# Optimization experiments

Hardware: AMD Instinct MI355X
Metric: run time of the kernel (lower is better)

Reference implementation:

```python
import jax, jax.numpy as jnp
import numpy as np

BITS = 8
TOPK_PERCENT = 0.1
THRESHOLD = 0.5


def _quantize_per_channel(v, n_bits):
    # scales: abs-max over last dim, clamped, divided by q_max
    q_max = 2 ** (n_bits - 1) - 1
    scales = jnp.max(jnp.abs(v), axis=-1, keepdims=True)
    scales = jnp.clip(scales, 1e-5, None) / q_max
    return jnp.clip(jnp.round(v / scales), -q_max - 1, q_max) * scales


def setup_inputs() -> dict:
    key = jax.random.key(0)
    ks = jax.random.split(key, 5)
    B, S, D, H = 4, 2048, 1024, 4096
    return {
        "x": jax.random.normal(ks[0], (B, S, D), dtype=jnp.float32),
        "W1": jax.random.normal(ks[1], (H, D), dtype=jnp.float32) * 0.02,
        "b1": jax.random.normal(ks[2], (H,), dtype=jnp.float32) * 0.02,
        "W2": jax.random.normal(ks[3], (D, H), dtype=jnp.float32) * 0.02,
        "b2": jax.random.normal(ks[4], (D,), dtype=jnp.float32) * 0.02,
    }


def reference(x, W1, b1, W2, b2):
    D = W1.shape[-1]
    H = W1.shape[0]
    topk_rows = int(D * TOPK_PERCENT) + 1  # first-k-columns approximation

    # approximate preactivation using only the first topk_rows input channels
    prod_topk = jnp.einsum('bsk,hk->bsh', x[:, :, :topk_rows], W1[:, :topk_rows]) + b1
    # exact fp preactivation
    prod = jnp.einsum('bsd,hd->bsh', x, W1) + b1

    # quantized path: per-channel quant of x, W1, b1 then matmul
    q_x = _quantize_per_channel(x, BITS)
    q_w = _quantize_per_channel(W1, BITS)
    q_b = _quantize_per_channel(b1, BITS)
    q_pre = jnp.einsum('bsd,hd->bsh', q_x, q_w) + q_b

    # channel selection: channels predicted positive often enough stay fp
    threshold = prod_topk.shape[-1] * THRESHOLD
    num_pos_pred = jnp.sum(prod_topk > 0, axis=(0, 1))  # [H]
    fp_channels = num_pos_pred > threshold              # [H] bool

    h = jnp.where(fp_channels, prod, q_pre)
    h = jax.nn.gelu(h, approximate=False)
    out = jnp.einsum('bsh,dh->bsd', h, W2) + b2
    return out
```

## Files before the change

### kernel.cpp

```cpp
#include <hip/hip_runtime.h>
#include <math.h>
#include <stdint.h>


typedef __bf16 v8bf __attribute__((ext_vector_type(8)));
typedef float v4f __attribute__((ext_vector_type(4)));
typedef unsigned short v8us __attribute__((ext_vector_type(8)));

#define AS_G __attribute__((address_space(1)))
#define AS_L __attribute__((address_space(3)))

__device__ __forceinline__ unsigned short f2bf(float f) {
    union { float f; unsigned int i; } v; v.f = f;
    unsigned int r = v.i + 0x7fffu + ((v.i >> 16) & 1u);
    return (unsigned short)(r >> 16);
}
__device__ __forceinline__ float gelu_fast(float v) {
    float u = v * (0.79788456080286536f + 0.035677408136300125f * v * v);
    u = fminf(fmaxf(u, -15.f), 15.f);
    float e = __expf(2.0f * u);
    return v * e * __builtin_amdgcn_rcpf(e + 1.0f);
}
__device__ __forceinline__ float gelu_exact(float v) {
    return 0.5f * v * (1.0f + erff(v * 0.70710678118654752440f));
}

__device__ __forceinline__ void gemm_core(const unsigned short* __restrict__ A,
                                          const unsigned short* __restrict__ B,
                                          int K, int bm0, int bn0,
                                          unsigned short* lds,
                                          v4f acc[4][4])
{
    const int tid  = threadIdx.x;
    const int wave = tid >> 6;
    const int lane = tid & 63;
    const int rowInChunk = lane >> 2;
    const int col8 = ((lane & 3) ^ ((lane >> 3) & 3)) * 8;
    const int ldsLane = lane * 8;
    const int c0 = wave * 2, c1 = wave * 2 + 1;
    const int wm = wave & 1, wn = wave >> 1;

    unsigned short* ldsA = lds;
    unsigned short* ldsB = lds + 4096;

    const size_t aR0 = (size_t)(bm0 + c0 * 16 + rowInChunk) * K + col8;
    const size_t aR1 = (size_t)(bm0 + c1 * 16 + rowInChunk) * K + col8;
    const size_t bR0 = (size_t)(bn0 + c0 * 16 + rowInChunk) * K + col8;
    const size_t bR1 = (size_t)(bn0 + c1 * 16 + rowInChunk) * K + col8;

    const int R = lane & 15, Q = lane >> 4;
    const int roff = R * 32 + ((Q ^ ((R >> 1) & 3)) * 8);

    for (int k0 = 0; k0 < K; k0 += 32) {
        __builtin_amdgcn_global_load_lds((const AS_G void*)(A + aR0 + k0),
                                         (AS_L void*)(ldsA + c0 * 512 + ldsLane), 16, 0, 0);
        __builtin_amdgcn_global_load_lds((const AS_G void*)(A + aR1 + k0),
                                         (AS_L void*)(ldsA + c1 * 512 + ldsLane), 16, 0, 0);
        __builtin_amdgcn_global_load_lds((const AS_G void*)(B + bR0 + k0),
                                         (AS_L void*)(ldsB + c0 * 512 + ldsLane), 16, 0, 0);
        __builtin_amdgcn_global_load_lds((const AS_G void*)(B + bR1 + k0),
                                         (AS_L void*)(ldsB + c1 * 512 + ldsLane), 16, 0, 0);
        __syncthreads();

        v8bf af[4], bfr[4];
#pragma unroll
        for (int i = 0; i < 4; ++i)
            af[i] = *(const v8bf*)&ldsA[(wm * 4 + i) * 512 + roff];
#pragma unroll
        for (int j = 0; j < 4; ++j)
            bfr[j] = *(const v8bf*)&ldsB[(wn * 4 + j) * 512 + roff];
#pragma unroll
        for (int i = 0; i < 4; ++i)
#pragma unroll
            for (int j = 0; j < 4; ++j)
                acc[i][j] = __builtin_amdgcn_mfma_f32_16x16x32_bf16(af[i], bfr[j], acc[i][j], 0, 0, 0);
        __syncthreads();
    }
}

__device__ __forceinline__ void gemm_core64N(const unsigned short* __restrict__ A,
                                             const unsigned short* __restrict__ B,
                                             int K, int bm0, int bn0,
                                             unsigned short* lds,
                                             v4f acc[4][2])
{
    const int tid  = threadIdx.x;
    const int wave = tid >> 6;
    const int lane = tid & 63;
    const int rowInChunk = lane >> 2;
    const int col8 = ((lane & 3) ^ ((lane >> 3) & 3)) * 8;
    const int ldsLane = lane * 8;
    const int c0 = wave * 2, c1 = wave * 2 + 1;
    const int wm = wave & 1, wn = wave >> 1;

    unsigned short* ldsA = lds;
    unsigned short* ldsB = lds + 4096;

    const size_t aR0 = (size_t)(bm0 + c0 * 16 + rowInChunk) * K + col8;
    const size_t aR1 = (size_t)(bm0 + c1 * 16 + rowInChunk) * K + col8;
    const size_t bR  = (size_t)(bn0 + wave * 16 + rowInChunk) * K + col8;

    const int R = lane & 15, Q = lane >> 4;
    const int roff = R * 32 + ((Q ^ ((R >> 1) & 3)) * 8);

    for (int k0 = 0; k0 < K; k0 += 32) {
        __builtin_amdgcn_global_load_lds((const AS_G void*)(A + aR0 + k0),
                                         (AS_L void*)(ldsA + c0 * 512 + ldsLane), 16, 0, 0);
        __builtin_amdgcn_global_load_lds((const AS_G void*)(A + aR1 + k0),
                                         (AS_L void*)(ldsA + c1 * 512 + ldsLane), 16, 0, 0);
        __builtin_amdgcn_global_load_lds((const AS_G void*)(B + bR + k0),
                                         (AS_L void*)(ldsB + wave * 512 + ldsLane), 16, 0, 0);
        __syncthreads();

        v8bf af[4], bfr[2];
#pragma unroll
        for (int i = 0; i < 4; ++i)
            af[i] = *(const v8bf*)&ldsA[(wm * 4 + i) * 512 + roff];
#pragma unroll
        for (int j = 0; j < 2; ++j)
            bfr[j] = *(const v8bf*)&ldsB[(wn * 2 + j) * 512 + roff];
#pragma unroll
        for (int i = 0; i < 4; ++i)
#pragma unroll
            for (int j = 0; j < 2; ++j)
                acc[i][j] = __builtin_amdgcn_mfma_f32_16x16x32_bf16(af[i], bfr[j], acc[i][j], 0, 0, 0);
        __syncthreads();
    }
}

__global__ void prep_kernel(const float* __restrict__ x, const float* __restrict__ W1,
                            const float* __restrict__ W2, const float* __restrict__ b1,
                            unsigned short* __restrict__ xb, unsigned short* __restrict__ w1b,
                            unsigned short* __restrict__ w2b,
                            unsigned short* __restrict__ xpad, unsigned short* __restrict__ w1pad,
                            float* __restrict__ s_x, float* __restrict__ s_w,
                            float* __restrict__ s_b, int* __restrict__ counts)
{
    const int b = blockIdx.x, t = threadIdx.x;
    __shared__ float red[4];

    if (b < 16384) {
        const float* src; unsigned short* dst; unsigned short* pad = nullptr; float* sc = nullptr;
        if (b < 8192)       { src = x  + (size_t)b * 1024;            dst = xb  + (size_t)b * 1024;
                              pad = xpad  + (size_t)b * 128;          sc = s_x + b; }
        else if (b < 12288) { int r = b - 8192;  src = W1 + (size_t)r * 1024; dst = w1b + (size_t)r * 1024;
                              pad = w1pad + (size_t)r * 128;          sc = s_w + r; }
        else                { int r = b - 12288; src = W2 + (size_t)r * 1024; dst = w2b + (size_t)r * 1024; }

        float4 v = ((const float4*)src)[t];
        ushort4 u;
        u.x = f2bf(v.x); u.y = f2bf(v.y); u.z = f2bf(v.z); u.w = f2bf(v.w);
        ((ushort4*)dst)[t] = u;
        if (pad && t < 32) {
            int c = t * 4;
            ushort4 p;
            p.x = (c + 0 < 103) ? u.x : (unsigned short)0;
            p.y = (c + 1 < 103) ? u.y : (unsigned short)0;
            p.z = (c + 2 < 103) ? u.z : (unsigned short)0;
            p.w = (c + 3 < 103) ? u.w : (unsigned short)0;
            ((ushort4*)pad)[t] = p;
        }
        if (sc) {
            float m = fmaxf(fmaxf(fabsf(v.x), fabsf(v.y)), fmaxf(fabsf(v.z), fabsf(v.w)));
#pragma unroll
            for (int off = 32; off; off >>= 1) m = fmaxf(m, __shfl_xor(m, off, 64));
            if ((t & 63) == 0) red[t >> 6] = m;
            __syncthreads();
            if (t == 0) {
                m = fmaxf(fmaxf(red[0], red[1]), fmaxf(red[2], red[3]));
                *sc = fmaxf(m, 1e-5f) * (1.0f / 127.0f);
            }
        }
    } else {
        float m = 0.f;
        for (int k = t; k < 4096; k += 256) { m = fmaxf(m, fabsf(b1[k])); counts[k] = 0; }
#pragma unroll
        for (int off = 32; off; off >>= 1) m = fmaxf(m, __shfl_xor(m, off, 64));
        if ((t & 63) == 0) red[t >> 6] = m;
        __syncthreads();
        if (t == 0) {
            m = fmaxf(fmaxf(red[0], red[1]), fmaxf(red[2], red[3]));
            *s_b = fmaxf(m, 1e-5f) * (1.0f / 127.0f);
        }
    }
}

__global__ __launch_bounds__(256, 4)
void gemm1_topk(const unsigned short* __restrict__ xb,
                const unsigned short* __restrict__ w1b,
                const unsigned short* __restrict__ xpad,
                const unsigned short* __restrict__ w1pad,
                const float* __restrict__ b1,
                unsigned short* __restrict__ hbuf,
                int* __restrict__ counts)
{
    __shared__ unsigned short lds[8192];
    v4f acc[4][4];
    v4f z = {0.f, 0.f, 0.f, 0.f};
#pragma unroll
    for (int i = 0; i < 4; ++i)
#pragma unroll
        for (int j = 0; j < 4; ++j) acc[i][j] = z;

    const int bm0 = blockIdx.x * 128, bn0 = blockIdx.y * 128;
    const int tid = threadIdx.x;
    const int lane = tid & 63, wave = tid >> 6;
    const int wm = wave & 1, wn = wave >> 1, q = lane >> 4;

    if (blockIdx.z == 0) {
        gemm_core(xb, w1b, 1024, bm0, bn0, lds, acc);

        float bvj[4];
#pragma unroll
        for (int j = 0; j < 4; ++j) bvj[j] = b1[bn0 + wn * 64 + j * 16 + (lane & 15)];

#pragma unroll
        for (int p = 0; p < 2; ++p) {
            __syncthreads();
            if (wm == p) {
#pragma unroll
                for (int j = 0; j < 4; ++j) {
                    int nl = wn * 64 + j * 16 + (lane & 15);
#pragma unroll
                    for (int i = 0; i < 4; ++i)
#pragma unroll
                        for (int r = 0; r < 4; ++r)
                            lds[(i * 16 + q * 4 + r) * 128 + nl] =
                                f2bf(gelu_fast(acc[i][j][r] + bvj[j]));
                }
            }
            __syncthreads();
#pragma unroll
            for (int s = 0; s < 4; ++s) {
                int c = s * 256 + tid;
                int row = c >> 4, ch = c & 15;
                *(v8us*)&hbuf[(size_t)(bm0 + p * 64 + row) * 4096 + bn0 + ch * 8] =
                    *(const v8us*)&lds[row * 128 + ch * 8];
            }
        }
    } else {
        gemm_core(xpad, w1pad, 128, bm0, bn0, lds, acc);

#pragma unroll
        for (int j = 0; j < 4; ++j) {
            int n = bn0 + wn * 64 + j * 16 + (lane & 15);
            float bv = b1[n];
            int cnt = 0;
#pragma unroll
            for (int i = 0; i < 4; ++i)
#pragma unroll
                for (int r = 0; r < 4; ++r)
                    cnt += (acc[i][j][r] + bv > 0.0f) ? 1 : 0;
            cnt += __shfl_xor(cnt, 16, 64);
            cnt += __shfl_xor(cnt, 32, 64);
            if (lane < 16 && cnt) atomicAdd(&counts[n], cnt);
        }
    }
}

__global__ void fixup_kernel(const float* __restrict__ x,
                             const float* __restrict__ W1,
                             const float* __restrict__ b1,
                             const int* __restrict__ counts,
                             const float* __restrict__ s_x,
                             const float* __restrict__ s_w,
                             const float* __restrict__ s_b,
                             unsigned short* __restrict__ hbuf)
{
    const int n = blockIdx.x;
    if (counts[n] > 2048) return;
    __shared__ float qw[1024];
    const float swn = s_w[n];
    for (int k = threadIdx.x; k < 1024; k += 256) {
        float q = nearbyintf(W1[(size_t)n * 1024 + k] / swn);
        qw[k] = fminf(fmaxf(q, -128.f), 127.f) * swn;
    }
    __syncthreads();
    const float sb = *s_b;
    const float bq = fminf(fmaxf(nearbyintf(b1[n] / sb), -128.f), 127.f) * sb;
    for (int m = threadIdx.x; m < 8192; m += 256) {
        const float sxm = s_x[m];
        float a = 0.f;
        for (int k = 0; k < 1024; ++k) {
            float q = nearbyintf(x[(size_t)m * 1024 + k] / sxm);
            a += fminf(fmaxf(q, -128.f), 127.f) * sxm * qw[k];
        }
        hbuf[(size_t)m * 4096 + n] = f2bf(gelu_exact(a + bq));
    }
}

__global__ __launch_bounds__(256, 4)
void gemm2_bias(const unsigned short* __restrict__ hbuf,
                const unsigned short* __restrict__ w2b,
                const float* __restrict__ b2,
                float* __restrict__ out)
{
    __shared__ unsigned short lds[6144];
    v4f acc[4][2];
    v4f z = {0.f, 0.f, 0.f, 0.f};
#pragma unroll
    for (int i = 0; i < 4; ++i)
#pragma unroll
        for (int j = 0; j < 2; ++j) acc[i][j] = z;

    const int bm0 = blockIdx.x * 128, bn0 = blockIdx.y * 64;
    gemm_core64N(hbuf, w2b, 4096, bm0, bn0, lds, acc);

    const int tid = threadIdx.x;
    const int lane = tid & 63, wave = tid >> 6;
    const int wm = wave & 1, wn = wave >> 1, q = lane >> 4;
    float* ldsf = (float*)lds;

    float bvj[2];
#pragma unroll
    for (int j = 0; j < 2; ++j) bvj[j] = b2[bn0 + wn * 32 + j * 16 + (lane & 15)];

#pragma unroll
    for (int p = 0; p < 4; ++p) {
        __syncthreads();
        if (wm == (p >> 1)) {
            const int ibase = (p & 1) * 2;
#pragma unroll
            for (int ii = 0; ii < 2; ++ii) {
#pragma unroll
                for (int j = 0; j < 2; ++j) {
                    int nl = wn * 32 + j * 16 + (lane & 15);
#pragma unroll
                    for (int r = 0; r < 4; ++r)
                        ldsf[(ii * 16 + q * 4 + r) * 64 + nl] =
                            acc[ibase + ii][j][r] + bvj[j];
                }
            }
        }
        __syncthreads();
#pragma unroll
        for (int s = 0; s < 2; ++s) {
            int c = s * 256 + tid;
            int row = c >> 4, ch = c & 15;
            *(float4*)&out[(size_t)(bm0 + p * 32 + row) * 1024 + bn0 + ch * 4] =
                *(const float4*)&ldsf[row * 64 + ch * 4];
        }
    }
}

extern "C" void kernel_launch(void* const* d_in, const int* in_sizes, int n_in,
                              void* d_out, int out_size, void* d_ws, size_t ws_size,
                              hipStream_t stream)
{
    const float* x  = (const float*)d_in[0];
    const float* W1 = (const float*)d_in[1];
    const float* b1 = (const float*)d_in[2];
    const float* W2 = (const float*)d_in[3];
    const float* b2 = (const float*)d_in[4];
    float* out = (float*)d_out;

    unsigned short* xb  = (unsigned short*)d_out;
    unsigned short* w1b = (unsigned short*)d_out + (size_t)8192 * 1024;

    char* ws = (char*)d_ws;
    int*   counts = (int*)(ws + 0);
    float* s_x    = (float*)(ws + (64 << 10));
    float* s_w    = (float*)(ws + (96 << 10));
    float* s_b    = (float*)(ws + (112 << 10));
    unsigned short* xpad  = (unsigned short*)(ws + (1 << 20));
    unsigned short* w1pad = (unsigned short*)(ws + (3 << 20));
    unsigned short* w2b   = (unsigned short*)(ws + (4 << 20));
    unsigned short* hbuf  = (unsigned short*)(ws + (12 << 20));

    prep_kernel<<<16385, 256, 0, stream>>>(x, W1, W2, b1, xb, w1b, w2b,
                                           xpad, w1pad, s_x, s_w, s_b, counts);
    gemm1_topk<<<dim3(64, 32, 2), 256, 0, stream>>>(xb, w1b, xpad, w1pad, b1, hbuf, counts);
    fixup_kernel<<<4096, 256, 0, stream>>>(x, W1, b1, counts, s_x, s_w, s_b, hbuf);
    gemm2_bias<<<dim3(64, 16), 256, 0, stream>>>(hbuf, w2b, b2, out);
}
```

Baseline: 299.3 us.

## Move W2 bf16 conversion into gemm1 grid and split fixup over row chunks

The W2 fp32-to-bf16 conversion moves out of the prep kernel into an extra z-slice of the gemm1 launch, so it can overlap with the GEMM blocks and prep gets shorter. The fixup kernel grid gains a second dimension that splits the 8192 rows into 8 chunks, giving more parallel blocks for the rare quantized channels. This also drops the branch on pad and scale pointers in prep. It adds lightweight blocks to gemm1 that compete with the GEMM blocks for CU slots, and fixup now reloads the quantized W1 row once per chunk.

```diff
diff --git a/kernel.cpp b/kernel.cpp
--- a/kernel.cpp
+++ b/kernel.cpp
@@ -129,9 +129,8 @@
 }
 
 __global__ void prep_kernel(const float* __restrict__ x, const float* __restrict__ W1,
-                            const float* __restrict__ W2, const float* __restrict__ b1,
+                            const float* __restrict__ b1,
                             unsigned short* __restrict__ xb, unsigned short* __restrict__ w1b,
-                            unsigned short* __restrict__ w2b,
                             unsigned short* __restrict__ xpad, unsigned short* __restrict__ w1pad,
                             float* __restrict__ s_x, float* __restrict__ s_w,
                             float* __restrict__ s_b, int* __restrict__ counts)
@@ -139,19 +138,18 @@
     const int b = blockIdx.x, t = threadIdx.x;
     __shared__ float red[4];
 
-    if (b < 16384) {
-        const float* src; unsigned short* dst; unsigned short* pad = nullptr; float* sc = nullptr;
-        if (b < 8192)       { src = x  + (size_t)b * 1024;            dst = xb  + (size_t)b * 1024;
-                              pad = xpad  + (size_t)b * 128;          sc = s_x + b; }
-        else if (b < 12288) { int r = b - 8192;  src = W1 + (size_t)r * 1024; dst = w1b + (size_t)r * 1024;
-                              pad = w1pad + (size_t)r * 128;          sc = s_w + r; }
-        else                { int r = b - 12288; src = W2 + (size_t)r * 1024; dst = w2b + (size_t)r * 1024; }
+    if (b < 12288) {
+        const float* src; unsigned short* dst; unsigned short* pad; float* sc;
+        if (b < 8192) { src = x  + (size_t)b * 1024;            dst = xb  + (size_t)b * 1024;
+                        pad = xpad  + (size_t)b * 128;          sc = s_x + b; }
+        else          { int r = b - 8192;  src = W1 + (size_t)r * 1024; dst = w1b + (size_t)r * 1024;
+                        pad = w1pad + (size_t)r * 128;          sc = s_w + r; }
 
         float4 v = ((const float4*)src)[t];
         ushort4 u;
         u.x = f2bf(v.x); u.y = f2bf(v.y); u.z = f2bf(v.z); u.w = f2bf(v.w);
         ((ushort4*)dst)[t] = u;
-        if (pad && t < 32) {
+        if (t < 32) {
             int c = t * 4;
             ushort4 p;
             p.x = (c + 0 < 103) ? u.x : (unsigned short)0;
@@ -160,16 +158,14 @@
             p.w = (c + 3 < 103) ? u.w : (unsigned short)0;
             ((ushort4*)pad)[t] = p;
         }
-        if (sc) {
-            float m = fmaxf(fmaxf(fabsf(v.x), fabsf(v.y)), fmaxf(fabsf(v.z), fabsf(v.w)));
-#pragma unroll
-            for (int off = 32; off; off >>= 1) m = fmaxf(m, __shfl_xor(m, off, 64));
-            if ((t & 63) == 0) red[t >> 6] = m;
-            __syncthreads();
-            if (t == 0) {
-                m = fmaxf(fmaxf(red[0], red[1]), fmaxf(red[2], red[3]));
-                *sc = fmaxf(m, 1e-5f) * (1.0f / 127.0f);
-            }
+        float m = fmaxf(fmaxf(fabsf(v.x), fabsf(v.y)), fmaxf(fabsf(v.z), fabsf(v.w)));
+#pragma unroll
+        for (int off = 32; off; off >>= 1) m = fmaxf(m, __shfl_xor(m, off, 64));
+        if ((t & 63) == 0) red[t >> 6] = m;
+        __syncthreads();
+        if (t == 0) {
+            m = fmaxf(fmaxf(red[0], red[1]), fmaxf(red[2], red[3]));
+            *sc = fmaxf(m, 1e-5f) * (1.0f / 127.0f);
         }
     } else {
         float m = 0.f;
@@ -191,10 +187,28 @@
                 const unsigned short* __restrict__ xpad,
                 const unsigned short* __restrict__ w1pad,
                 const float* __restrict__ b1,
+                const float* __restrict__ W2,
+                unsigned short* __restrict__ w2b,
                 unsigned short* __restrict__ hbuf,
                 int* __restrict__ counts)
 {
     __shared__ unsigned short lds[8192];
+    const int tid = threadIdx.x;
+
+    if (blockIdx.z == 2) {
+        const int r = (blockIdx.y * 64 + (int)blockIdx.x) * 2;
+        const float* src = W2 + (size_t)r * 1024;
+        unsigned short* dst = w2b + (size_t)r * 1024;
+#pragma unroll
+        for (int h = 0; h < 2; ++h) {
+            float4 v = ((const float4*)src)[tid + h * 256];
+            ushort4 u;
+            u.x = f2bf(v.x); u.y = f2bf(v.y); u.z = f2bf(v.z); u.w = f2bf(v.w);
+            ((ushort4*)dst)[tid + h * 256] = u;
+        }
+        return;
+    }
+
     v4f acc[4][4];
     v4f z = {0.f, 0.f, 0.f, 0.f};
 #pragma unroll
@@ -203,7 +217,6 @@
         for (int j = 0; j < 4; ++j) acc[i][j] = z;
 
     const int bm0 = blockIdx.x * 128, bn0 = blockIdx.y * 128;
-    const int tid = threadIdx.x;
     const int lane = tid & 63, wave = tid >> 6;
     const int wm = wave & 1, wn = wave >> 1, q = lane >> 4;
 
@@ -278,7 +291,8 @@
     __syncthreads();
     const float sb = *s_b;
     const float bq = fminf(fmaxf(nearbyintf(b1[n] / sb), -128.f), 127.f) * sb;
-    for (int m = threadIdx.x; m < 8192; m += 256) {
+    const int m0 = blockIdx.y * 1024;
+    for (int m = m0 + threadIdx.x; m < m0 + 1024; m += 256) {
         const float sxm = s_x[m];
         float a = 0.f;
         for (int k = 0; k < 1024; ++k) {
@@ -367,9 +381,10 @@
     unsigned short* w2b   = (unsigned short*)(ws + (4 << 20));
     unsigned short* hbuf  = (unsigned short*)(ws + (12 << 20));
 
-    prep_kernel<<<16385, 256, 0, stream>>>(x, W1, W2, b1, xb, w1b, w2b,
+    prep_kernel<<<12289, 256, 0, stream>>>(x, W1, b1, xb, w1b,
                                            xpad, w1pad, s_x, s_w, s_b, counts);
-    gemm1_topk<<<dim3(64, 32, 2), 256, 0, stream>>>(xb, w1b, xpad, w1pad, b1, hbuf, counts);
-    fixup_kernel<<<4096, 256, 0, stream>>>(x, W1, b1, counts, s_x, s_w, s_b, hbuf);
+    gemm1_topk<<<dim3(64, 32, 3), 256, 0, stream>>>(xb, w1b, xpad, w1pad, b1,
+                                                    W2, w2b, hbuf, counts);
+    fixup_kernel<<<dim3(4096, 8), 256, 0, stream>>>(x, W1, b1, counts, s_x, s_w, s_b, hbuf);
     gemm2_bias<<<dim3(64, 16), 256, 0, stream>>>(hbuf, w2b, b2, out);
 }
```

New measurement: 317.8 us. 6.2% more time.

## Double-buffer LDS in both GEMM cores to overlap global loads with MFMA

Applied to the files above, without the earlier changes.

Both GEMM inner loops now use two LDS stages. The next K-tile is issued via global_load_lds into the alternate buffer before the current tile's MFMAs run, which removes one of the two barriers per iteration. The MFMA block is wrapped in s_setprio to favor math waves. This doubles the LDS per block (32KB and 24KB), which may limit occupancy under launch_bounds(256,4). It also depends on the single remaining barrier being enough to order the async LDS writes correctly.

```diff
diff --git a/kernel.cpp b/kernel.cpp
--- a/kernel.cpp
+++ b/kernel.cpp
@@ -9,6 +9,7 @@
 
 #define AS_G __attribute__((address_space(1)))
 #define AS_L __attribute__((address_space(3)))
+#define GLOAD(gp, lp) __builtin_amdgcn_global_load_lds((const AS_G void*)(gp), (AS_L void*)(lp), 16, 0, 0)
 
 __device__ __forceinline__ unsigned short f2bf(float f) {
     union { float f; unsigned int i; } v; v.f = f;
@@ -40,9 +41,6 @@
     const int c0 = wave * 2, c1 = wave * 2 + 1;
     const int wm = wave & 1, wn = wave >> 1;
 
-    unsigned short* ldsA = lds;
-    unsigned short* ldsB = lds + 4096;
-
     const size_t aR0 = (size_t)(bm0 + c0 * 16 + rowInChunk) * K + col8;
     const size_t aR1 = (size_t)(bm0 + c1 * 16 + rowInChunk) * K + col8;
     const size_t bR0 = (size_t)(bn0 + c0 * 16 + rowInChunk) * K + col8;
@@ -50,32 +48,40 @@
 
     const int R = lane & 15, Q = lane >> 4;
     const int roff = R * 32 + ((Q ^ ((R >> 1) & 3)) * 8);
-
-    for (int k0 = 0; k0 < K; k0 += 32) {
-        __builtin_amdgcn_global_load_lds((const AS_G void*)(A + aR0 + k0),
-                                         (AS_L void*)(ldsA + c0 * 512 + ldsLane), 16, 0, 0);
-        __builtin_amdgcn_global_load_lds((const AS_G void*)(A + aR1 + k0),
-                                         (AS_L void*)(ldsA + c1 * 512 + ldsLane), 16, 0, 0);
-        __builtin_amdgcn_global_load_lds((const AS_G void*)(B + bR0 + k0),
-                                         (AS_L void*)(ldsB + c0 * 512 + ldsLane), 16, 0, 0);
-        __builtin_amdgcn_global_load_lds((const AS_G void*)(B + bR1 + k0),
-                                         (AS_L void*)(ldsB + c1 * 512 + ldsLane), 16, 0, 0);
-        __syncthreads();
+    const int NT = K >> 5;
+
+#define G1_STG(t, bp) { const int kk_ = (t) << 5;                              \
+        GLOAD(A + aR0 + kk_, (bp) + c0 * 512 + ldsLane);                       \
+        GLOAD(A + aR1 + kk_, (bp) + c1 * 512 + ldsLane);                       \
+        GLOAD(B + bR0 + kk_, (bp) + 4096 + c0 * 512 + ldsLane);                \
+        GLOAD(B + bR1 + kk_, (bp) + 4096 + c1 * 512 + ldsLane); }
+
+    G1_STG(0, lds);
+    __syncthreads();
+
+    for (int t = 0; t < NT; ++t) {
+        unsigned short* cur = lds + (t & 1) * 8192;
+        unsigned short* nxt = lds + ((t + 1) & 1) * 8192;
+        if (t + 1 < NT) { G1_STG(t + 1, nxt); }
+        __builtin_amdgcn_sched_barrier(0);
 
         v8bf af[4], bfr[4];
 #pragma unroll
         for (int i = 0; i < 4; ++i)
-            af[i] = *(const v8bf*)&ldsA[(wm * 4 + i) * 512 + roff];
+            af[i] = *(const v8bf*)&cur[(wm * 4 + i) * 512 + roff];
 #pragma unroll
         for (int j = 0; j < 4; ++j)
-            bfr[j] = *(const v8bf*)&ldsB[(wn * 4 + j) * 512 + roff];
+            bfr[j] = *(const v8bf*)&cur[4096 + (wn * 4 + j) * 512 + roff];
+        __builtin_amdgcn_s_setprio(1);
 #pragma unroll
         for (int i = 0; i < 4; ++i)
 #pragma unroll
             for (int j = 0; j < 4; ++j)
                 acc[i][j] = __builtin_amdgcn_mfma_f32_16x16x32_bf16(af[i], bfr[j], acc[i][j], 0, 0, 0);
-        __syncthreads();
-    }
+        __builtin_amdgcn_s_setprio(0);
+        __syncthreads();
+    }
+#undef G1_STG
 }
 
 __device__ __forceinline__ void gemm_core64N(const unsigned short* __restrict__ A,
@@ -93,39 +99,45 @@
     const int c0 = wave * 2, c1 = wave * 2 + 1;
     const int wm = wave & 1, wn = wave >> 1;
 
-    unsigned short* ldsA = lds;
-    unsigned short* ldsB = lds + 4096;
-
     const size_t aR0 = (size_t)(bm0 + c0 * 16 + rowInChunk) * K + col8;
     const size_t aR1 = (size_t)(bm0 + c1 * 16 + rowInChunk) * K + col8;
     const size_t bR  = (size_t)(bn0 + wave * 16 + rowInChunk) * K + col8;
 
     const int R = lane & 15, Q = lane >> 4;
     const int roff = R * 32 + ((Q ^ ((R >> 1) & 3)) * 8);
-
-    for (int k0 = 0; k0 < K; k0 += 32) {
-        __builtin_amdgcn_global_load_lds((const AS_G void*)(A + aR0 + k0),
-                                         (AS_L void*)(ldsA + c0 * 512 + ldsLane), 16, 0, 0);
-        __builtin_amdgcn_global_load_lds((const AS_G void*)(A + aR1 + k0),
-                                         (AS_L void*)(ldsA + c1 * 512 + ldsLane), 16, 0, 0);
-        __builtin_amdgcn_global_load_lds((const AS_G void*)(B + bR + k0),
-                                         (AS_L void*)(ldsB + wave * 512 + ldsLane), 16, 0, 0);
-        __syncthreads();
+    const int NT = K >> 5;
+
+#define G2_STG(t, bp) { const int kk_ = (t) << 5;                              \
+        GLOAD(A + aR0 + kk_, (bp) + c0 * 512 + ldsLane);                       \
+        GLOAD(A + aR1 + kk_, (bp) + c1 * 512 + ldsLane);                       \
+        GLOAD(B + bR  + kk_, (bp) + 4096 + wave * 512 + ldsLane); }
+
+    G2_STG(0, lds);
+    __syncthreads();
+
+    for (int t = 0; t < NT; ++t) {
+        unsigned short* cur = lds + (t & 1) * 6144;
+        unsigned short* nxt = lds + ((t + 1) & 1) * 6144;
+        if (t + 1 < NT) { G2_STG(t + 1, nxt); }
+        __builtin_amdgcn_sched_barrier(0);
 
         v8bf af[4], bfr[2];
 #pragma unroll
         for (int i = 0; i < 4; ++i)
-            af[i] = *(const v8bf*)&ldsA[(wm * 4 + i) * 512 + roff];
+            af[i] = *(const v8bf*)&cur[(wm * 4 + i) * 512 + roff];
 #pragma unroll
         for (int j = 0; j < 2; ++j)
-            bfr[j] = *(const v8bf*)&ldsB[(wn * 2 + j) * 512 + roff];
+            bfr[j] = *(const v8bf*)&cur[4096 + (wn * 2 + j) * 512 + roff];
+        __builtin_amdgcn_s_setprio(1);
 #pragma unroll
         for (int i = 0; i < 4; ++i)
 #pragma unroll
             for (int j = 0; j < 2; ++j)
                 acc[i][j] = __builtin_amdgcn_mfma_f32_16x16x32_bf16(af[i], bfr[j], acc[i][j], 0, 0, 0);
-        __syncthreads();
-    }
+        __builtin_amdgcn_s_setprio(0);
+        __syncthreads();
+    }
+#undef G2_STG
 }
 
 __global__ void prep_kernel(const float* __restrict__ x, const float* __restrict__ W1,
@@ -194,7 +206,7 @@
                 unsigned short* __restrict__ hbuf,
                 int* __restrict__ counts)
 {
-    __shared__ unsigned short lds[8192];
+    __shared__ unsigned short lds[16384];
     v4f acc[4][4];
     v4f z = {0.f, 0.f, 0.f, 0.f};
 #pragma unroll
@@ -295,7 +307,7 @@
                 const float* __restrict__ b2,
                 float* __restrict__ out)
 {
-    __shared__ unsigned short lds[6144];
+    __shared__ unsigned short lds[12288];
     v4f acc[4][2];
     v4f z = {0.f, 0.f, 0.f, 0.f};
 #pragma unroll
```

New measurement: 300.3 us. About the same (+0.3%).
